# Kernel optimization log

Measured on AMD Instinct MI355X. Metric: run time of the kernel, lower is better.

## Reference

```python
import jax, jax.numpy as jnp
import numpy as np

PAD = (2, 2)  # from kernel=[1,3,3,1], sampling_factor_padding=2, kernel_size=3


def _make_kernel(k1d):
    k = np.asarray(k1d, dtype=np.float32)
    k2d = k[None, :] * k[:, None]
    return jnp.asarray(k2d / k2d.sum())


def setup_inputs() -> dict:
    key = jax.random.key(0)
    x = jax.random.normal(key, (8, 256, 256, 256), dtype=jnp.float32)
    kernel = _make_kernel([1, 3, 3, 1])  # [4,4] normalized FIR kernel (buffer)
    return {"x": x, "kernel": kernel}


def reference(x, kernel):
    # upfirdn2d with up=1, down=1, pad=(2,2): pad then depthwise TRUE convolution
    # (StyleGAN2 flips the kernel before F.conv2d, i.e. real convolution).
    B, C, H, W = x.shape
    kh, kw = kernel.shape
    w = jnp.flip(kernel, (0, 1)).astype(x.dtype)[None, None]  # [1,1,kh,kw]
    w = jnp.broadcast_to(w, (C, 1, kh, kw))  # depthwise: same kernel per channel
    out = jax.lax.conv_general_dilated(
        x, w,
        window_strides=(1, 1),
        padding=(PAD, PAD),
        dimension_numbers=("NCHW", "OIHW", "NCHW"),
        feature_group_count=C,
    )  # [B, C, H+1, W+1] since H + 4 - 4 + 1 = H + 1
    return out
```

## Files before the change

### kernel.cpp

```cpp
#include <hip/hip_runtime.h>


#define IW 256
#define IH 256
#define OW 257
#define OH 257
#define NG 65

typedef float f4u __attribute__((vector_size(16), aligned(4)));

__device__ __forceinline__ float sbc(float v) {
    return __uint_as_float(__builtin_amdgcn_readfirstlane(__float_as_uint(v)));
}

__global__ __launch_bounds__(256) void blur_fir_kernel(
    const float* __restrict__ x,
    const float* __restrict__ k2d,
    float* __restrict__ out,
    int ntasks, int nwaves)
{
    const int lane = threadIdx.x & 63;
    const int gw   = (blockIdx.x << 2) + (threadIdx.x >> 6);

    const float w0 = sbc(k2d[0]);
    const float w1 = sbc(k2d[1]);
    const float w2 = sbc(k2d[2]);
    const float w3 = sbc(k2d[3]);
    const float inv = 1.0f / w0;
    const float v1 = sbc(k2d[4]  * inv);
    const float v2 = sbc(k2d[8]  * inv);
    const float v3 = sbc(k2d[12] * inv);

    const int   c0 = lane << 2;
    const float mL = (lane > 0)  ? 1.0f : 0.0f;
    const float mR = (lane < 63) ? 1.0f : 0.0f;
    const int   lm = (lane > 0)  ? lane - 1 : 0;
    const int   lp = (lane < 63) ? lane + 1 : 63;
    const bool last = (lane == 63);

    for (int t = gw; t < ntasks; t += nwaves) {
        const int plane = t / NG;
        const int rg    = t - plane * NG;
        const float* xp = x + ((size_t)plane << 16);
        float* op = out + (size_t)plane * (OW * OH) + (size_t)(rg << 2) * OW + c0;

        auto loadraw = [&](int r) -> float4 {
            int rr = min(max(r, 0), IH - 1);
            return *(const float4*)(xp + (rr << 8) + c0);
        };
        auto hcomb = [&](float4 Bv, int r, float4& h, float& h4) {
            float rm = (r >= 0 && r < IH) ? 1.0f : 0.0f;
            float lx = __shfl(Bv.z, lm, 64) * mL;
            float ly = __shfl(Bv.w, lm, 64) * mL;
            float rv = __shfl(Bv.x, lp, 64) * mR;
            h.x = w0 * Bv.y + w1 * Bv.x + w2 * ly   + w3 * lx;
            h.y = w0 * Bv.z + w1 * Bv.y + w2 * Bv.x + w3 * ly;
            h.z = w0 * Bv.w + w1 * Bv.z + w2 * Bv.y + w3 * Bv.x;
            h.w = w0 * rv   + w1 * Bv.w + w2 * Bv.z + w3 * Bv.y;
            h4  = w2 * Bv.w + w3 * Bv.z;
            h.x *= rm; h.y *= rm; h.z *= rm; h.w *= rm; h4 *= rm;
        };
        auto vcomb = [&](float4 a, float4 b, float4 c, float4 d) -> float4 {
            float4 r;
            r.x = a.x + v1 * b.x + v2 * c.x + v3 * d.x;
            r.y = a.y + v1 * b.y + v2 * c.y + v3 * d.y;
            r.z = a.z + v1 * b.z + v2 * c.z + v3 * d.z;
            r.w = a.w + v1 * b.w + v2 * c.w + v3 * d.w;
            return r;
        };

        if (rg < 64) {
            const int rb = rg << 2;
            float4 G0 = loadraw(rb - 2), G1 = loadraw(rb - 1), G2 = loadraw(rb);
            float4 G3 = loadraw(rb + 1), G4 = loadraw(rb + 2), G5 = loadraw(rb + 3);
            float4 G6 = loadraw(rb + 4);

            float4 F0, F1, F2, F3, F4, F5, F6;
            float  s0, s1, s2, s3, s4, s5, s6;
            hcomb(G0, rb - 2, F0, s0);
            hcomb(G1, rb - 1, F1, s1);
            hcomb(G2, rb    , F2, s2);
            hcomb(G3, rb + 1, F3, s3);
            hcomb(G4, rb + 2, F4, s4);
            hcomb(G5, rb + 3, F5, s5);
            hcomb(G6, rb + 4, F6, s6);

            float4 R0 = vcomb(F3, F2, F1, F0);
            float4 R1 = vcomb(F4, F3, F2, F1);
            float4 R2 = vcomb(F5, F4, F3, F2);
            float4 R3 = vcomb(F6, F5, F4, F3);
            *(f4u*)(op         ) = (f4u){R0.x, R0.y, R0.z, R0.w};
            *(f4u*)(op +     OW) = (f4u){R1.x, R1.y, R1.z, R1.w};
            *(f4u*)(op + 2 * OW) = (f4u){R2.x, R2.y, R2.z, R2.w};
            *(f4u*)(op + 3 * OW) = (f4u){R3.x, R3.y, R3.z, R3.w};
            if (last) {
                op[4]          = s3 + v1 * s2 + v2 * s1 + v3 * s0;
                op[OW + 4]     = s4 + v1 * s3 + v2 * s2 + v3 * s1;
                op[2 * OW + 4] = s5 + v1 * s4 + v2 * s3 + v3 * s2;
                op[3 * OW + 4] = s6 + v1 * s5 + v2 * s4 + v3 * s3;
            }
        } else {
            float4 GA = loadraw(254), GB = loadraw(255);
            float4 FA, FB; float sA, sB;
            hcomb(GA, 254, FA, sA);
            hcomb(GB, 255, FB, sB);
            float4 R;
            R.x = v2 * FB.x + v3 * FA.x;
            R.y = v2 * FB.y + v3 * FA.y;
            R.z = v2 * FB.z + v3 * FA.z;
            R.w = v2 * FB.w + v3 * FA.w;
            *(f4u*)op = (f4u){R.x, R.y, R.z, R.w};
            if (last) op[4] = v2 * sB + v3 * sA;
        }
    }
}

extern "C" void kernel_launch(void* const* d_in, const int* in_sizes, int n_in,
                              void* d_out, int out_size, void* d_ws, size_t ws_size,
                              hipStream_t stream) {
    const float* x   = (const float*)d_in[0];
    const float* k2d = (const float*)d_in[1];
    float* out = (float*)d_out;

    int nplanes = in_sizes[0] >> 16;
    int ntasks  = nplanes * NG;
    int nblocks = 2048;
    int nwaves  = nblocks * 4;

    blur_fir_kernel<<<nblocks, 256, 0, stream>>>(x, k2d, out, ntasks, nwaves);
}
```

Measured before the change: 234.6 us.

## Share horizontally filtered rows across block waves via LDS to cut halo reloads

```diff
diff --git a/kernel.cpp b/kernel.cpp
--- a/kernel.cpp
+++ b/kernel.cpp
@@ -5,7 +5,8 @@
 #define IH 256
 #define OW 257
 #define OH 257
-#define NG 65
+#define HSTR 260
+#define NSLOT 19
 
 typedef float f4u __attribute__((vector_size(16), aligned(4)));
 
@@ -17,10 +18,12 @@
     const float* __restrict__ x,
     const float* __restrict__ k2d,
     float* __restrict__ out,
-    int ntasks, int nwaves)
+    int ntasks, int nstride)
 {
+    __shared__ float Hs[NSLOT * HSTR];
+
     const int lane = threadIdx.x & 63;
-    const int gw   = (blockIdx.x << 2) + (threadIdx.x >> 6);
+    const int wv   = threadIdx.x >> 6;
 
     const float w0 = sbc(k2d[0]);
     const float w1 = sbc(k2d[1]);
@@ -38,79 +41,87 @@
     const int   lp = (lane < 63) ? lane + 1 : 63;
     const bool last = (lane == 63);
 
-    for (int t = gw; t < ntasks; t += nwaves) {
-        const int plane = t / NG;
-        const int rg    = t - plane * NG;
+    for (int t = blockIdx.x; t < ntasks; t += nstride) {
+        const int plane = t >> 4;
+        const int rg    = t & 15;
+        const int a     = rg << 4;
         const float* xp = x + ((size_t)plane << 16);
-        float* op = out + (size_t)plane * (OW * OH) + (size_t)(rg << 2) * OW + c0;
 
-        auto loadraw = [&](int r) -> float4 {
+        __syncthreads();
+
+        #pragma unroll
+        for (int j = wv; j < NSLOT; j += 4) {
+            const int r = a - 2 + j;
             int rr = min(max(r, 0), IH - 1);
-            return *(const float4*)(xp + (rr << 8) + c0);
-        };
-        auto hcomb = [&](float4 Bv, int r, float4& h, float& h4) {
+            float4 Bv = *(const float4*)(xp + (rr << 8) + c0);
             float rm = (r >= 0 && r < IH) ? 1.0f : 0.0f;
             float lx = __shfl(Bv.z, lm, 64) * mL;
             float ly = __shfl(Bv.w, lm, 64) * mL;
             float rv = __shfl(Bv.x, lp, 64) * mR;
+            float4 h;
             h.x = w0 * Bv.y + w1 * Bv.x + w2 * ly   + w3 * lx;
             h.y = w0 * Bv.z + w1 * Bv.y + w2 * Bv.x + w3 * ly;
             h.z = w0 * Bv.w + w1 * Bv.z + w2 * Bv.y + w3 * Bv.x;
             h.w = w0 * rv   + w1 * Bv.w + w2 * Bv.z + w3 * Bv.y;
-            h4  = w2 * Bv.w + w3 * Bv.z;
-            h.x *= rm; h.y *= rm; h.z *= rm; h.w *= rm; h4 *= rm;
-        };
-        auto vcomb = [&](float4 a, float4 b, float4 c, float4 d) -> float4 {
+            float h4 = (w2 * Bv.w + w3 * Bv.z) * rm;
+            h.x *= rm; h.y *= rm; h.z *= rm; h.w *= rm;
+            float* hp = Hs + j * HSTR;
+            *(float4*)(hp + c0) = h;
+            if (last) hp[256] = h4;
+        }
+        __syncthreads();
+
+        const int j0 = wv << 2;
+        const float* hb = Hs + j0 * HSTR + c0;
+        float4 h0 = *(const float4*)(hb           );
+        float4 h1 = *(const float4*)(hb +     HSTR);
+        float4 h2 = *(const float4*)(hb + 2 * HSTR);
+        float4 h3 = *(const float4*)(hb + 3 * HSTR);
+        float4 h4 = *(const float4*)(hb + 4 * HSTR);
+        float4 h5 = *(const float4*)(hb + 5 * HSTR);
+        float4 h6 = *(const float4*)(hb + 6 * HSTR);
+
+        auto vcomb = [&](float4 A, float4 B, float4 C, float4 D) -> float4 {
             float4 r;
-            r.x = a.x + v1 * b.x + v2 * c.x + v3 * d.x;
-            r.y = a.y + v1 * b.y + v2 * c.y + v3 * d.y;
-            r.z = a.z + v1 * b.z + v2 * c.z + v3 * d.z;
-            r.w = a.w + v1 * b.w + v2 * c.w + v3 * d.w;
+            r.x = A.x + v1 * B.x + v2 * C.x + v3 * D.x;
+            r.y = A.y + v1 * B.y + v2 * C.y + v3 * D.y;
+            r.z = A.z + v1 * B.z + v2 * C.z + v3 * D.z;
+            r.w = A.w + v1 * B.w + v2 * C.w + v3 * D.w;
             return r;
         };
 
-        if (rg < 64) {
-            const int rb = rg << 2;
-            float4 G0 = loadraw(rb - 2), G1 = loadraw(rb - 1), G2 = loadraw(rb);
-            float4 G3 = loadraw(rb + 1), G4 = loadraw(rb + 2), G5 = loadraw(rb + 3);
-            float4 G6 = loadraw(rb + 4);
+        float* op = out + (size_t)plane * (OW * OH)
+                        + (size_t)(a + (wv << 2)) * OW + c0;
+        float4 R0 = vcomb(h3, h2, h1, h0);
+        float4 R1 = vcomb(h4, h3, h2, h1);
+        float4 R2 = vcomb(h5, h4, h3, h2);
+        float4 R3 = vcomb(h6, h5, h4, h3);
+        *(f4u*)(op         ) = (f4u){R0.x, R0.y, R0.z, R0.w};
+        *(f4u*)(op +     OW) = (f4u){R1.x, R1.y, R1.z, R1.w};
+        *(f4u*)(op + 2 * OW) = (f4u){R2.x, R2.y, R2.z, R2.w};
+        *(f4u*)(op + 3 * OW) = (f4u){R3.x, R3.y, R3.z, R3.w};
+        if (last) {
+            const float* sp = Hs + j0 * HSTR + 256;
+            float s0 = sp[0],        s1 = sp[HSTR],     s2 = sp[2 * HSTR];
+            float s3 = sp[3 * HSTR], s4 = sp[4 * HSTR], s5 = sp[5 * HSTR];
+            float s6 = sp[6 * HSTR];
+            op[4]          = s3 + v1 * s2 + v2 * s1 + v3 * s0;
+            op[OW + 4]     = s4 + v1 * s3 + v2 * s2 + v3 * s1;
+            op[2 * OW + 4] = s5 + v1 * s4 + v2 * s3 + v3 * s2;
+            op[3 * OW + 4] = s6 + v1 * s5 + v2 * s4 + v3 * s3;
+        }
 
-            float4 F0, F1, F2, F3, F4, F5, F6;
-            float  s0, s1, s2, s3, s4, s5, s6;
-            hcomb(G0, rb - 2, F0, s0);
-            hcomb(G1, rb - 1, F1, s1);
-            hcomb(G2, rb    , F2, s2);
-            hcomb(G3, rb + 1, F3, s3);
-            hcomb(G4, rb + 2, F4, s4);
-            hcomb(G5, rb + 3, F5, s5);
-            hcomb(G6, rb + 4, F6, s6);
-
-            float4 R0 = vcomb(F3, F2, F1, F0);
-            float4 R1 = vcomb(F4, F3, F2, F1);
-            float4 R2 = vcomb(F5, F4, F3, F2);
-            float4 R3 = vcomb(F6, F5, F4, F3);
-            *(f4u*)(op         ) = (f4u){R0.x, R0.y, R0.z, R0.w};
-            *(f4u*)(op +     OW) = (f4u){R1.x, R1.y, R1.z, R1.w};
-            *(f4u*)(op + 2 * OW) = (f4u){R2.x, R2.y, R2.z, R2.w};
-            *(f4u*)(op + 3 * OW) = (f4u){R3.x, R3.y, R3.z, R3.w};
-            if (last) {
-                op[4]          = s3 + v1 * s2 + v2 * s1 + v3 * s0;
-                op[OW + 4]     = s4 + v1 * s3 + v2 * s2 + v3 * s1;
-                op[2 * OW + 4] = s5 + v1 * s4 + v2 * s3 + v3 * s2;
-                op[3 * OW + 4] = s6 + v1 * s5 + v2 * s4 + v3 * s3;
-            }
-        } else {
-            float4 GA = loadraw(254), GB = loadraw(255);
-            float4 FA, FB; float sA, sB;
-            hcomb(GA, 254, FA, sA);
-            hcomb(GB, 255, FB, sB);
+        if (rg == 15 && wv == 3) {
+            float4 Hm2 = *(const float4*)(Hs + 16 * HSTR + c0);
+            float4 Hm1 = *(const float4*)(Hs + 17 * HSTR + c0);
             float4 R;
-            R.x = v2 * FB.x + v3 * FA.x;
-            R.y = v2 * FB.y + v3 * FA.y;
-            R.z = v2 * FB.z + v3 * FA.z;
-            R.w = v2 * FB.w + v3 * FA.w;
-            *(f4u*)op = (f4u){R.x, R.y, R.z, R.w};
-            if (last) op[4] = v2 * sB + v3 * sA;
+            R.x = v2 * Hm1.x + v3 * Hm2.x;
+            R.y = v2 * Hm1.y + v3 * Hm2.y;
+            R.z = v2 * Hm1.z + v3 * Hm2.z;
+            R.w = v2 * Hm1.w + v3 * Hm2.w;
+            *(f4u*)(op + 4 * OW) = (f4u){R.x, R.y, R.z, R.w};
+            if (last)
+                op[4 * OW + 4] = v2 * Hs[17 * HSTR + 256] + v3 * Hs[16 * HSTR + 256];
         }
     }
 }
@@ -123,9 +134,8 @@
     float* out = (float*)d_out;
 
     int nplanes = in_sizes[0] >> 16;
-    int ntasks  = nplanes * NG;
+    int ntasks  = nplanes * 16;
     int nblocks = 2048;
-    int nwaves  = nblocks * 4;
 
-    blur_fir_kernel<<<nblocks, 256, 0, stream>>>(x, k2d, out, ntasks, nwaves);
+    blur_fir_kernel<<<nblocks, 256, 0, stream>>>(x, k2d, out, ntasks, nblocks);
 }
```

After: 217.6 us. 1.08x faster.
